# Optimization experiments

Measured on AMD Instinct MI355X. Metric: run time of the kernel, lower is better.

Reference implementation:

```python
import jax, jax.numpy as jnp
import numpy as np

N_NEG = 60
TEMP = 0.07

def _normalize(x, axis):
    n = jnp.sqrt(jnp.sum(x * x, axis=axis, keepdims=True))
    return x / jnp.maximum(n, 1e-12)

def _grid_sample(img, grid):
    # img [B,C,H,W], grid [B,h,w,2] in [-1,1]; bilinear, padding_mode='border', align_corners=False
    B, C, H, W = img.shape
    ix = jnp.clip((grid[..., 0] + 1.0) * (W * 0.5) - 0.5, 0.0, W - 1.0)
    iy = jnp.clip((grid[..., 1] + 1.0) * (H * 0.5) - 0.5, 0.0, H - 1.0)
    x0 = jnp.floor(ix); y0 = jnp.floor(iy)
    x1 = jnp.minimum(x0 + 1.0, W - 1.0); y1 = jnp.minimum(y0 + 1.0, H - 1.0)
    wx = (ix - x0)[:, None]; wy = (iy - y0)[:, None]  # [B,1,h,w]
    imgf = img.reshape(B, C, H * W)
    hh, ww = grid.shape[1], grid.shape[2]
    def gat(yy, xx):
        idx = (yy * W + xx).astype(jnp.int32).reshape(B, 1, hh * ww)
        return jnp.take_along_axis(imgf, idx, axis=2).reshape(B, C, hh, ww)
    v00 = gat(y0, x0); v01 = gat(y0, x1); v10 = gat(y1, x0); v11 = gat(y1, x1)
    return (v00 * (1 - wx) * (1 - wy) + v01 * wx * (1 - wy)
            + v10 * (1 - wx) * wy + v11 * wx * wy)

def _forward(ref_fms, tgt_fms, target_l, target_r, queue):
    b, c, h, w = ref_fms.shape
    s = target_l.shape[-1] // w  # integer downscale factor (nearest interpolate == strided slice)
    disps_l = target_l[:, :, ::s, ::s] / float(s)   # [b,1,h,w]
    disps_r = target_r[:, :, ::s, ::s] / float(s)
    xb = jnp.broadcast_to(jnp.linspace(0.0, 1.0, w), (b, h, w))
    yb = jnp.broadcast_to(jnp.linspace(0.0, 1.0, h)[:, None], (b, h, w))

    def warp(img, disp):
        g = jnp.stack([xb + disp[:, 0] / w, yb], axis=-1)
        return _grid_sample(img, 2.0 * g - 1.0)

    # occlusion / validity mask (detached in the original)
    index = jnp.broadcast_to(jnp.arange(w, dtype=ref_fms.dtype), (b, 1, h, w))
    l2r2l = warp(warp(index, disps_r), -disps_l)
    masko = jnp.abs(index - l2r2l)[:, 0] < 3.0
    mask = masko & (disps_l[:, 0] > 0.0) & (xb - disps_l[:, 0] / w >= 0.0)
    mask = jax.lax.stop_gradient(mask).astype(ref_fms.dtype)  # [b,h,w]

    query = _normalize(ref_fms, 1)
    # positive: warp right feature to left view via disparity
    gpos = jnp.stack([xb - disps_l[:, 0] / w, yb], axis=-1)
    positive = _normalize(_grid_sample(tgt_fms, 2.0 * gpos - 1.0), 1)
    l_pos = jnp.einsum('bchw,bchw->bhw', query, positive)[..., None]

    # negatives: random integer pixel shifts around positive location
    # (no n_neg-fold repeat of tgt_fms; vmap grid_sample over the n axis instead)
    k1, k2 = jax.random.split(jax.random.key(1234))
    mag = jax.random.randint(k1, (b, h, w, N_NEG), 1, 25).astype(ref_fms.dtype)
    sgn = jnp.sign(jax.random.uniform(k2, (b, h, w, N_NEG)) - 0.5).astype(ref_fms.dtype)
    x_right = (xb - disps_l[:, 0] / w) * w
    fx = jnp.mod(x_right[..., None] + mag * sgn, float(w)) / w
    fy = fx / h  # faithful to original code (y coord reuses the normalized x coord)
    grids = jnp.moveaxis(jnp.stack([fx, fy], axis=-1), 3, 0)  # [n,b,h,w,2]
    neg = jax.vmap(lambda g: _grid_sample(tgt_fms, 2.0 * g - 1.0))(grids)  # [n,b,c,h,w]
    neg = _normalize(jnp.moveaxis(neg, 0, -1), 1)  # [b,c,h,w,n]
    l_neg = jnp.einsum('bchw,bchwn->bhwn', query, neg)

    qn = _normalize(queue, 0)  # forward re-normalizes the queue each call
    l_q = jnp.einsum('bchw,ck->bhwk', query, jax.lax.stop_gradient(qn))

    logits = jnp.concatenate([l_pos, l_neg, l_q], axis=-1) * mask[..., None]
    logits = logits.reshape(b * h * w, -1) / TEMP
    # CrossEntropyLoss with all-zero labels (positive is class 0)
    return jnp.mean(-jax.nn.log_softmax(logits, axis=-1)[:, 0])

def setup_inputs():
    key = jax.random.key(0)
    k1, k2, k3, k4, k5 = jax.random.split(key, 5)
    b, c, h, w = 2, 128, 64, 128
    H, W = 4 * h, 4 * w
    return {
        'ref_fms': jax.random.normal(k1, (b, c, h, w), jnp.float32),
        'tgt_fms': jax.random.normal(k2, (b, c, h, w), jnp.float32),
        'target_l': jax.random.uniform(k3, (b, 1, H, W), jnp.float32) * 64.0,
        'target_r': jax.random.uniform(k4, (b, 1, H, W), jnp.float32) * 64.0,
        'queue': jax.random.normal(k5, (c, 6000), jnp.float32),
    }

def reference(ref_fms, tgt_fms, target_l, target_r, queue):
    return _forward(ref_fms, tgt_fms, target_l, target_r, queue)
```

## Files before the change

kernel.cpp:

```cpp
#include <hip/hip_runtime.h>
#include <stdint.h>
#include <math.h>

#define HFM 64
#define WFM 128
#define CFM 128
#define BN 2
#define HWFM (HFM*WFM)
#define NPIX (BN*HWFM)
#define KQ 6000
#define KQP 6144
#define NNEG 60
#define NE (NPIX*NNEG)
#define EHALF_U 491520u
#define MSHIFT 15.0f
#define LOG2E 1.4426950408889634f
#define BSTRIDE 136

typedef _Float16 f16_8 __attribute__((ext_vector_type(8)));
typedef _Float16 f16_2 __attribute__((ext_vector_type(2)));
typedef float f32_4 __attribute__((ext_vector_type(4)));

__host__ __device__ __forceinline__ void threefry2x32(uint32_t k0, uint32_t k1,
                                                      uint32_t x0, uint32_t x1,
                                                      uint32_t* o0, uint32_t* o1) {
  uint32_t ks2 = k0 ^ k1 ^ 0x1BD11BDAu;
  x0 += k0; x1 += k1;
#define TFR(r) { x0 += x1; x1 = (x1 << (r)) | (x1 >> (32 - (r))); x1 ^= x0; }
  TFR(13) TFR(15) TFR(26) TFR(6)
  x0 += k1;  x1 += ks2 + 1u;
  TFR(17) TFR(29) TFR(16) TFR(24)
  x0 += ks2; x1 += k0 + 2u;
  TFR(13) TFR(15) TFR(26) TFR(6)
  x0 += k0;  x1 += k1 + 3u;
  TFR(17) TFR(29) TFR(16) TFR(24)
  x0 += k1;  x1 += ks2 + 4u;
  TFR(13) TFR(15) TFR(26) TFR(6)
  x0 += ks2; x1 += k0 + 5u;
#undef TFR
  *o0 = x0; *o1 = x1;
}

__device__ __forceinline__ void gs_coord(float t, float halfdim, float maxc,
                                         int* i0, int* i1, float* w) {
  float g = 2.0f * t - 1.0f;
  float x = (g + 1.0f) * halfdim - 0.5f;
  x = fminf(fmaxf(x, 0.0f), maxc);
  float f = floorf(x);
  *i0 = (int)f;
  *w = x - f;
  *i1 = (int)fminf(f + 1.0f, maxc);
}

__global__ __launch_bounds__(256) void k_A(
    const float* __restrict__ ref, const float* __restrict__ tgt,
    const float* __restrict__ queue,
    const float* __restrict__ target_l, const float* __restrict__ target_r,
    _Float16* __restrict__ refTf, _Float16* __restrict__ tgtTf,
    _Float16* __restrict__ queueTf, float2* __restrict__ qeb,
    float* __restrict__ maskArr, float* __restrict__ xr) {
  __shared__ float tile[32][33];
  int blk = blockIdx.x;
  int tid = threadIdx.x;
  if (blk < 4096) {
    int z = blk >> 10, yb_ = (blk >> 8) & 3, xb_ = blk & 255;
    int arr = z >> 1, b = z & 1;
    const float* src = (arr == 0 ? ref : tgt) + (size_t)b * CFM * HWFM;
    _Float16* dst = (arr == 0 ? refTf : tgtTf) + (size_t)b * HWFM * CFM;
    int x0 = xb_ * 32, y0 = yb_ * 32;
    int tx = tid & 31, ty = tid >> 5;
#pragma unroll
    for (int i = 0; i < 32; i += 8)
      tile[ty + i][tx] = src[(size_t)(y0 + ty + i) * HWFM + x0 + tx];
    __syncthreads();
#pragma unroll
    for (int i = 0; i < 32; i += 8)
      dst[(size_t)(x0 + ty + i) * CFM + (y0 + tx)] = (_Float16)tile[tx][ty + i];
  } else if (blk < 4864) {
    int q = blk - 4096;
    int cy = q / 192, nx = q - cy * 192;
    int n0 = nx * 32, c0 = cy * 32;
    int tx = tid & 31, ty = tid >> 5;
#pragma unroll
    for (int i = 0; i < 32; i += 8) {
      int n = n0 + tx;
      tile[ty + i][tx] = (n < KQ) ? queue[(size_t)(c0 + ty + i) * KQ + n] : 0.0f;
    }
    __syncthreads();
#pragma unroll
    for (int i = 0; i < 32; i += 8)
      queueTf[(size_t)(n0 + ty + i) * CFM + (c0 + tx)] = (_Float16)tile[tx][ty + i];
  } else if (blk < 4888) {
    int k = (blk - 4864) * 256 + tid;
    if (k < KQP) {
      if (k >= KQ) { qeb[k] = make_float2(0.0f, -1000.0f); }
      else {
        float ss = 0.0f;
        for (int c = 0; c < CFM; c++) { float v = queue[c * KQ + k]; ss += v * v; }
        float qi = 1.0f / fmaxf(sqrtf(ss), 1e-12f);
        qeb[k] = make_float2(qi * (LOG2E / 0.07f), -MSHIFT * LOG2E);
      }
    }
  } else {
    int p = (blk - 4888) * 256 + tid;
    int b = p >> 13;
    int rem = p & (HWFM - 1);
    int i = rem >> 7, j = rem & 127;
    const float stepx = 1.0f / 127.0f, stepy = 1.0f / 63.0f;
    float xb = (j == 127) ? 1.0f : j * stepx;
    float yb = (i == 63) ? 1.0f : i * stepy;
    const float* tl = target_l + (size_t)b * 256 * 512;
    const float* tr = target_r + (size_t)b * 256 * 512;
    float dl = tl[(4 * i) * 512 + 4 * j] * 0.25f;
    int y0i, y1i; float wy;
    gs_coord(yb, 32.0f, 63.0f, &y0i, &y1i, &wy);
    float t = xb - dl * (1.0f / 128.0f);
    int x0i, x1i; float wx;
    gs_coord(t, 64.0f, 127.0f, &x0i, &x1i, &wx);
    auto innerv = [&](int y, int x) -> float {
      float xbx = (x == 127) ? 1.0f : x * stepx;
      float drv = tr[(4 * y) * 512 + 4 * x] * 0.25f;
      float ti = xbx + drv * (1.0f / 128.0f);
      float g = 2.0f * ti - 1.0f;
      float ix2 = fminf(fmaxf((g + 1.0f) * 64.0f - 0.5f, 0.0f), 127.0f);
      float x0f = floorf(ix2);
      float wxp = ix2 - x0f;
      float x1f = fminf(x0f + 1.0f, 127.0f);
      return x0f * (1.0f - wxp) + x1f * wxp;
    };
    float v00 = innerv(y0i, x0i), v01 = innerv(y0i, x1i);
    float v10 = innerv(y1i, x0i), v11 = innerv(y1i, x1i);
    float l2r2l = v00 * (1.0f - wx) * (1.0f - wy) + v01 * wx * (1.0f - wy)
                + v10 * (1.0f - wx) * wy + v11 * wx * wy;
    bool masko = fabsf((float)j - l2r2l) < 3.0f;
    bool mk = masko && (dl > 0.0f) && (t >= 0.0f);
    maskArr[p] = mk ? 1.0f : 0.0f;
    xr[p] = t * 128.0f;
  }
}

__global__ __launch_bounds__(256) void k_compact(const float* __restrict__ maskArr,
                                                 int* __restrict__ count,
                                                 int* __restrict__ list) {
  __shared__ int wsum[4];
  int tid = threadIdx.x;
  int lane = tid & 63, wave = tid >> 6;
  int base_p = tid * 64;
  unsigned long long bits = 0ull;
  const float4* m4 = (const float4*)(maskArr + base_p);
#pragma unroll
  for (int k = 0; k < 16; k++) {
    float4 v = m4[k];
    if (v.x > 0.0f) bits |= 1ull << (4 * k + 0);
    if (v.y > 0.0f) bits |= 1ull << (4 * k + 1);
    if (v.z > 0.0f) bits |= 1ull << (4 * k + 2);
    if (v.w > 0.0f) bits |= 1ull << (4 * k + 3);
  }
  int m = __popcll(bits);
  int scan = m;
#pragma unroll
  for (int off = 1; off < 64; off <<= 1) {
    int n = __shfl_up(scan, off, 64);
    if (lane >= off) scan += n;
  }
  if (lane == 63) wsum[wave] = scan;
  __syncthreads();
  int wbase = 0;
  for (int w = 0; w < wave; w++) wbase += wsum[w];
  int idx = wbase + scan - m;
  for (int k = 0; k < 64; k++) {
    if ((bits >> k) & 1ull) list[idx++] = base_p + k;
  }
  if (tid == 255) *count = idx;
}

__global__ __launch_bounds__(256) void k_B(
    const _Float16* __restrict__ refTf, const _Float16* __restrict__ tgtTf,
    _Float16* __restrict__ QTfc, float* __restrict__ stats,
    const float* __restrict__ maskArr, const float* __restrict__ xr,
    float* __restrict__ S, float* __restrict__ logit0,
    const int* __restrict__ count, const int* __restrict__ list) {
  int blk = blockIdx.x;
  int tid = threadIdx.x;
  int lane = tid & 63;
  if (blk < 64) {
    int sub = tid >> 6;
    int xg = blk * 4 + sub;
    int b = xg >> 7, x = xg & 127;
    int xp = min(x + 1, 127);
    int c2 = lane * 2;
    int base = b * HWFM;
    f16_2 c0  = *(const f16_2*)(tgtTf + (size_t)(base + x) * CFM + c2);
    f16_2 c1  = *(const f16_2*)(tgtTf + (size_t)(base + WFM + x) * CFM + c2);
    f16_2 c0p = *(const f16_2*)(tgtTf + (size_t)(base + xp) * CFM + c2);
    f16_2 c1p = *(const f16_2*)(tgtTf + (size_t)(base + WFM + xp) * CFM + c2);
    float a0 = (float)c0[0], a1 = (float)c0[1];
    float b0 = (float)c1[0], b1 = (float)c1[1];
    float p0 = (float)c0p[0], p1 = (float)c0p[1];
    float q0 = (float)c1p[0], q1 = (float)c1p[1];
    float s[7];
    s[0] = a0 * a0 + a1 * a1;
    s[1] = a0 * b0 + a1 * b1;
    s[2] = b0 * b0 + b1 * b1;
    s[3] = a0 * p0 + a1 * p1;
    s[4] = a0 * q0 + a1 * q1;
    s[5] = b0 * p0 + b1 * p1;
    s[6] = b0 * q0 + b1 * q1;
#pragma unroll
    for (int o = 32; o; o >>= 1)
#pragma unroll
      for (int k = 0; k < 7; k++) s[k] += __shfl_xor(s[k], o, 64);
    if (lane == 0) {
      float* st = stats + (size_t)xg * 8;
#pragma unroll
      for (int k = 0; k < 7; k++) st[k] = s[k];
      st[7] = 0.0f;
    }
  } else {
    int wave = tid >> 6;
    int cnt = *count;
    int slot = (blk - 64) * 4 + wave;
    if (slot >= cnt) return;
    int p = list[slot];
    int b = p >> 13;
    int rem = p & (HWFM - 1);
    int i = rem >> 7;
    const float stepy = 1.0f / 63.0f;
    float yb = (i == 63) ? 1.0f : i * stepy;
    float t = xr[p] * (1.0f / 128.0f);
    int y0i, y1i; float wy;
    gs_coord(yb, 32.0f, 63.0f, &y0i, &y1i, &wy);
    int x0i, x1i; float wx;
    gs_coord(t, 64.0f, 127.0f, &x0i, &x1i, &wx);

    int c2 = lane * 2;
    f16_2 q2 = *(const f16_2*)(refTf + (size_t)p * CFM + c2);
    int bo = b * HWFM;
    f16_2 a2 = *(const f16_2*)(tgtTf + (size_t)(bo + y0i * WFM + x0i) * CFM + c2);
    f16_2 b2 = *(const f16_2*)(tgtTf + (size_t)(bo + y0i * WFM + x1i) * CFM + c2);
    f16_2 cc2 = *(const f16_2*)(tgtTf + (size_t)(bo + y1i * WFM + x0i) * CFM + c2);
    f16_2 d2 = *(const f16_2*)(tgtTf + (size_t)(bo + y1i * WFM + x1i) * CFM + c2);

    float w00 = (1.0f - wx) * (1.0f - wy), w01 = wx * (1.0f - wy);
    float w10 = (1.0f - wx) * wy,          w11 = wx * wy;
    float q0 = (float)q2[0], q1 = (float)q2[1];
    float v0 = w00 * (float)a2[0] + w01 * (float)b2[0] + w10 * (float)cc2[0] + w11 * (float)d2[0];
    float v1 = w00 * (float)a2[1] + w01 * (float)b2[1] + w10 * (float)cc2[1] + w11 * (float)d2[1];

    float s0 = q0 * q0 + q1 * q1;
    float s1 = q0 * v0 + q1 * v1;
    float s2 = v0 * v0 + v1 * v1;
#pragma unroll
    for (int o = 32; o; o >>= 1) {
      s0 += __shfl_xor(s0, o, 64);
      s1 += __shfl_xor(s1, o, 64);
      s2 += __shfl_xor(s2, o, 64);
    }
    float inv = 1.0f / fmaxf(sqrtf(s0), 1e-12f);
    f16_2 qw; qw[0] = (_Float16)(q0 * inv); qw[1] = (_Float16)(q1 * inv);
    *(f16_2*)(QTfc + (size_t)slot * CFM + c2) = qw;
    if (lane == 0) {
      float lpos = (s1 * inv) / fmaxf(sqrtf(s2), 1e-12f);
      float lg0 = lpos / 0.07f;
      logit0[p] = lg0;
      S[p] = expf(lg0 - MSHIFT);
    }
  }
}

__global__ __launch_bounds__(256) void k_gemm(
    const _Float16* __restrict__ QTfc,
    const _Float16* __restrict__ queueTf,
    const _Float16* __restrict__ tgtTf,
    const float2* __restrict__ qeb,
    float* __restrict__ S, float* __restrict__ D,
    const int* __restrict__ count, const int* __restrict__ list) {
  __shared__ _Float16 Bs[128 * BSTRIDE];
  __shared__ float Srow[64];
  __shared__ int pb[64];
  int tid = threadIdx.x;
  int cnt = *count;
  int pblk = blockIdx.y * 64;
  if (pblk >= cnt) return;
  int wave = tid >> 6, lane = tid & 63;
  int quad = lane >> 4, l16 = lane & 15;
  int wm = wave >> 1, wn = wave & 1;

  if (tid < 64) {
    Srow[tid] = 0.0f;
    pb[tid] = list[min(pblk + tid, cnt - 1)] >> 13;
  }

  f16_8 Af[2][4];
  int r0 = pblk + wm * 32;
#pragma unroll
  for (int mt = 0; mt < 2; mt++) {
    const _Float16* arow = QTfc + (size_t)min(r0 + mt * 16 + l16, cnt - 1) * CFM + quad * 8;
#pragma unroll
    for (int ks = 0; ks < 4; ks++)
      Af[mt][ks] = *(const f16_8*)(arow + ks * 32);
  }

  if (blockIdx.x < 4) {
    int batch = blockIdx.x >> 1;
    const _Float16* bsrc = tgtTf + ((size_t)batch * HWFM + (blockIdx.x & 1) * 128) * CFM;
#pragma unroll
    for (int it = 0; it < 8; it++) {
      int idx = it * 256 + tid;
      int row = idx >> 4, c16 = idx & 15;
      *(f16_8*)(&Bs[row * BSTRIDE + c16 * 8]) =
          *(const f16_8*)(bsrc + (size_t)row * CFM + c16 * 8);
    }
    __syncthreads();

    f32_4 acc[2][4];
#pragma unroll
    for (int mt = 0; mt < 2; mt++)
#pragma unroll
      for (int nt = 0; nt < 4; nt++)
        acc[mt][nt] = (f32_4){0.0f, 0.0f, 0.0f, 0.0f};
#pragma unroll
    for (int ks = 0; ks < 4; ks++) {
      f16_8 Bk[4];
#pragma unroll
      for (int nt = 0; nt < 4; nt++)
        Bk[nt] = *(const f16_8*)(&Bs[(wn * 64 + nt * 16 + l16) * BSTRIDE + ks * 32 + quad * 8]);
#pragma unroll
      for (int mt = 0; mt < 2; mt++)
#pragma unroll
        for (int nt = 0; nt < 4; nt++)
          acc[mt][nt] = __builtin_amdgcn_mfma_f32_16x16x32_f16(Af[mt][ks], Bk[nt], acc[mt][nt], 0, 0, 0);
    }
#pragma unroll
    for (int mt = 0; mt < 2; mt++)
#pragma unroll
      for (int nt = 0; nt < 4; nt++)
#pragma unroll
        for (int r = 0; r < 4; r++) {
          int rowloc = wm * 32 + mt * 16 + quad * 4 + r;
          int slot = pblk + rowloc;
          int colL = (blockIdx.x & 1) * 128 + wn * 64 + nt * 16 + l16;
          if (slot < cnt && pb[rowloc] == batch)
            D[(size_t)slot * 256 + colL] = acc[mt][nt][r];
        }
    __syncthreads();
  }

  float rowsum[2][4] = {{0.0f,0.0f,0.0f,0.0f},{0.0f,0.0f,0.0f,0.0f}};
#pragma unroll
  for (int ic = 0; ic < 4; ic++) {
    int n0 = (blockIdx.x * 4 + ic) * 128;
    {
      const _Float16* bsrc = queueTf + (size_t)n0 * CFM;
#pragma unroll
      for (int it = 0; it < 8; it++) {
        int idx = it * 256 + tid;
        int row = idx >> 4, c16 = idx & 15;
        *(f16_8*)(&Bs[row * BSTRIDE + c16 * 8]) =
            *(const f16_8*)(bsrc + (size_t)row * CFM + c16 * 8);
      }
    }
    float2 qb[4];
#pragma unroll
    for (int nt = 0; nt < 4; nt++) qb[nt] = qeb[n0 + wn * 64 + nt * 16 + l16];
    __syncthreads();

    f32_4 acc[2][4];
#pragma unroll
    for (int mt = 0; mt < 2; mt++)
#pragma unroll
      for (int nt = 0; nt < 4; nt++)
        acc[mt][nt] = (f32_4){0.0f, 0.0f, 0.0f, 0.0f};
#pragma unroll
    for (int ks = 0; ks < 4; ks++) {
      f16_8 Bk[4];
#pragma unroll
      for (int nt = 0; nt < 4; nt++)
        Bk[nt] = *(const f16_8*)(&Bs[(wn * 64 + nt * 16 + l16) * BSTRIDE + ks * 32 + quad * 8]);
#pragma unroll
      for (int mt = 0; mt < 2; mt++)
#pragma unroll
        for (int nt = 0; nt < 4; nt++)
          acc[mt][nt] = __builtin_amdgcn_mfma_f32_16x16x32_f16(Af[mt][ks], Bk[nt], acc[mt][nt], 0, 0, 0);
    }
#pragma unroll
    for (int nt = 0; nt < 4; nt++)
#pragma unroll
      for (int mt = 0; mt < 2; mt++)
#pragma unroll
        for (int r = 0; r < 4; r++)
          rowsum[mt][r] += exp2f(fmaf(acc[mt][nt][r], qb[nt].x, qb[nt].y));
    __syncthreads();
  }

#pragma unroll
  for (int mt = 0; mt < 2; mt++)
#pragma unroll
    for (int r = 0; r < 4; r++) {
      float vv = rowsum[mt][r];
      vv += __shfl_xor(vv, 1);
      vv += __shfl_xor(vv, 2);
      vv += __shfl_xor(vv, 4);
      vv += __shfl_xor(vv, 8);
      rowsum[mt][r] = vv;
    }
  if (l16 == 0) {
#pragma unroll
    for (int mt = 0; mt < 2; mt++)
#pragma unroll
      for (int r = 0; r < 4; r++)
        atomicAdd(&Srow[wm * 32 + mt * 16 + quad * 4 + r], rowsum[mt][r]);
  }
  __syncthreads();
  if (tid < 64) {
    int pr = pblk + tid;
    if (pr < cnt) atomicAdd(&S[list[pr]], Srow[tid]);
  }
}

__global__ __launch_bounds__(256) void k_negatives_lite(
    const float* __restrict__ D, const float* __restrict__ stats,
    const float* __restrict__ xr, float* __restrict__ S,
    const int* __restrict__ count, const int* __restrict__ list,
    uint32_t k1a, uint32_t k1b, uint32_t k2a, uint32_t k2b) {
  int tid = threadIdx.x;
  int wave = tid >> 6, lane = tid & 63;
  int cnt = *count;
  int slot = blockIdx.x * 4 + wave;
  if (slot >= cnt) return;
  int p = list[slot];
  int b = p >> 13;
  float esum = 0.0f;
  if (lane < NNEG) {
    uint32_t e = (uint32_t)(p * NNEG + lane);
    uint32_t h0, h1;
    threefry2x32(k1a, k1b, e, e + (uint32_t)NE, &h0, &h1);
    uint32_t off = ((h0 % 24u) * 16u + (h1 % 24u)) % 24u;
    float mag = (float)(1u + off);
    uint32_t ub;
    {
      uint32_t a, bm;
      if (e < EHALF_U) { threefry2x32(k2a, k2b, e, e + EHALF_U, &a, &bm); ub = a; }
      else             { threefry2x32(k2a, k2b, e - EHALF_U, e, &a, &bm); ub = bm; }
    }
    float u = __uint_as_float((ub >> 9) | 0x3F800000u) - 1.0f;
    float sg = (u > 0.5f) ? 1.0f : ((u < 0.5f) ? -1.0f : 0.0f);

    float v = xr[p] + mag * sg;
    float r = fmodf(v, 128.0f);
    if (r < 0.0f) r += 128.0f;
    float fx = r * (1.0f / 128.0f);
    float fy = fx * (1.0f / 64.0f);
    int x0i, x1i, y0i, y1i; float wx, wy;
    gs_coord(fx, 64.0f, 127.0f, &x0i, &x1i, &wx);
    gs_coord(fy, 32.0f, 63.0f, &y0i, &y1i, &wy);

    const float* Dp = D + (size_t)slot * 256;
    float d00 = Dp[x0i], d01 = Dp[x1i];
    float d10 = Dp[128 + x0i], d11 = Dp[128 + x1i];
    float u0 = 1.0f - wy, u1 = wy;
    float dv0 = u0 * d00 + u1 * d10;
    float dv1 = u0 * d01 + u1 * d11;
    float dot = (1.0f - wx) * dv0 + wx * dv1;

    const float* st0 = stats + (size_t)(b * 128 + x0i) * 8;
    const float* st1 = stats + (size_t)(b * 128 + x1i) * 8;
    float4 sa = *(const float4*)st0;
    float4 sb = *(const float4*)(st0 + 4);
    float4 sc = *(const float4*)st1;
    float a0 = u0 * u0, a1 = u0 * u1, a2 = u1 * u1;
    float nB0 = a0 * sa.x + 2.0f * a1 * sa.y + a2 * sa.z;
    float nB1 = a0 * sc.x + 2.0f * a1 * sc.y + a2 * sc.z;
    float cB  = a0 * sa.w + a1 * (sb.x + sb.y) + a2 * sb.z;
    float wx0 = 1.0f - wx;
    float nsq = wx0 * wx0 * nB0 + 2.0f * wx * wx0 * cB + wx * wx * nB1;
    float ln = dot / fmaxf(sqrtf(fmaxf(nsq, 0.0f)), 1e-12f);
    esum = __expf(ln * (1.0f / 0.07f) - MSHIFT);
  }
#pragma unroll
  for (int o = 32; o; o >>= 1) esum += __shfl_xor(esum, o, 64);
  if (lane == 0) atomicAdd(&S[p], esum);
}

__global__ __launch_bounds__(1024) void k_finalize(
    const float* __restrict__ S, const float* __restrict__ logit0,
    const float* __restrict__ maskArr, float* __restrict__ out) {
  int tid = threadIdx.x;
  const float cmask = logf(6061.0f);
  double acc = 0.0;
  for (int p = tid; p < NPIX; p += 1024) {
    float term = (maskArr[p] > 0.0f) ? (logf(S[p]) + MSHIFT - logit0[p]) : cmask;
    acc += (double)term;
  }
#pragma unroll
  for (int off = 32; off; off >>= 1) acc += __shfl_down(acc, off, 64);
  __shared__ double sd[16];
  if ((tid & 63) == 0) sd[tid >> 6] = acc;
  __syncthreads();
  if (tid == 0) {
    double tot = 0.0;
    for (int w = 0; w < 16; w++) tot += sd[w];
    out[0] = (float)(tot / (double)NPIX);
  }
}

extern "C" void kernel_launch(void* const* d_in, const int* in_sizes, int n_in,
                              void* d_out, int out_size, void* d_ws, size_t ws_size,
                              hipStream_t stream) {
  const float* ref   = (const float*)d_in[0];
  const float* tgt   = (const float*)d_in[1];
  const float* tl    = (const float*)d_in[2];
  const float* tr    = (const float*)d_in[3];
  const float* queue = (const float*)d_in[4];
  float* out = (float*)d_out;
  float* ws = (float*)d_ws;

  float2* qeb = (float2*)ws;
  float* S    = ws + 12288;
  float* lg0  = ws + 28672;
  float* mk   = ws + 45056;
  float* xr   = ws + 61440;
  int* count  = (int*)(ws + 77824);
  int* list   = (int*)(ws + 77840);
  _Float16* QTfc    = (_Float16*)(ws + 94464);
  _Float16* queueTf = (_Float16*)(ws + 1143040);
  _Float16* tgtTf   = (_Float16*)(ws + 1536256);
  _Float16* refTf   = (_Float16*)(ws + 2584832);
  float* stats = ws + 3633408;
  float* D     = ws + 3635456;

  uint32_t b0o0, b0o1, b1o0, b1o1;
  threefry2x32(0u, 1234u, 0u, 2u, &b0o0, &b0o1);
  threefry2x32(0u, 1234u, 1u, 3u, &b1o0, &b1o1);
  uint32_t k1a = b0o0, k1b = b1o0, k2a = b0o1, k2b = b1o1;

  k_A<<<dim3(4952), dim3(256), 0, stream>>>(ref, tgt, queue, tl, tr,
                                            refTf, tgtTf, queueTf, qeb, mk, xr);
  k_compact<<<dim3(1), dim3(256), 0, stream>>>(mk, count, list);
  k_B<<<dim3(64 + 4096), dim3(256), 0, stream>>>(refTf, tgtTf, QTfc, stats,
                                                 mk, xr, S, lg0, count, list);
  k_gemm<<<dim3(12, NPIX / 64), dim3(256), 0, stream>>>(QTfc, queueTf, tgtTf, qeb,
                                                        S, D, count, list);
  k_negatives_lite<<<dim3(NPIX / 4), dim3(256), 0, stream>>>(D, stats, xr, S, count, list,
                                                             k1a, k1b, k2a, k2b);
  k_finalize<<<dim3(1), dim3(1024), 0, stream>>>(S, lg0, mk, out);
}
```

Measured before the change: 137.4 us.

## Double-buffer queue tiles in GEMM, fold compaction into k_B, halve GEMM grid

The queue GEMM now prefetches the next 128-column B tile into registers while running MFMAs on the current tile, then writes it into a second LDS buffer. This removes one barrier per iteration and hides global-load latency. Each block now covers 8 chunks instead of 4, so the grid is halved. The separate compaction kernel is merged into k_B as block 0, and the normalized query rows are written per pixel using the mask directly. The GEMM then gathers its A rows through the list. In exchange, LDS use doubles, register pressure rises, there are fewer GEMM blocks for occupancy, and the A-row reads become indirect.

```diff
diff --git a/kernel.cpp b/kernel.cpp
--- a/kernel.cpp
+++ b/kernel.cpp
@@ -62,47 +62,8 @@
   __shared__ float tile[32][33];
   int blk = blockIdx.x;
   int tid = threadIdx.x;
-  if (blk < 4096) {
-    int z = blk >> 10, yb_ = (blk >> 8) & 3, xb_ = blk & 255;
-    int arr = z >> 1, b = z & 1;
-    const float* src = (arr == 0 ? ref : tgt) + (size_t)b * CFM * HWFM;
-    _Float16* dst = (arr == 0 ? refTf : tgtTf) + (size_t)b * HWFM * CFM;
-    int x0 = xb_ * 32, y0 = yb_ * 32;
-    int tx = tid & 31, ty = tid >> 5;
-#pragma unroll
-    for (int i = 0; i < 32; i += 8)
-      tile[ty + i][tx] = src[(size_t)(y0 + ty + i) * HWFM + x0 + tx];
-    __syncthreads();
-#pragma unroll
-    for (int i = 0; i < 32; i += 8)
-      dst[(size_t)(x0 + ty + i) * CFM + (y0 + tx)] = (_Float16)tile[tx][ty + i];
-  } else if (blk < 4864) {
-    int q = blk - 4096;
-    int cy = q / 192, nx = q - cy * 192;
-    int n0 = nx * 32, c0 = cy * 32;
-    int tx = tid & 31, ty = tid >> 5;
-#pragma unroll
-    for (int i = 0; i < 32; i += 8) {
-      int n = n0 + tx;
-      tile[ty + i][tx] = (n < KQ) ? queue[(size_t)(c0 + ty + i) * KQ + n] : 0.0f;
-    }
-    __syncthreads();
-#pragma unroll
-    for (int i = 0; i < 32; i += 8)
-      queueTf[(size_t)(n0 + ty + i) * CFM + (c0 + tx)] = (_Float16)tile[tx][ty + i];
-  } else if (blk < 4888) {
-    int k = (blk - 4864) * 256 + tid;
-    if (k < KQP) {
-      if (k >= KQ) { qeb[k] = make_float2(0.0f, -1000.0f); }
-      else {
-        float ss = 0.0f;
-        for (int c = 0; c < CFM; c++) { float v = queue[c * KQ + k]; ss += v * v; }
-        float qi = 1.0f / fmaxf(sqrtf(ss), 1e-12f);
-        qeb[k] = make_float2(qi * (LOG2E / 0.07f), -MSHIFT * LOG2E);
-      }
-    }
-  } else {
-    int p = (blk - 4888) * 256 + tid;
+  if (blk < 64) {
+    int p = blk * 256 + tid;
     int b = p >> 13;
     int rem = p & (HWFM - 1);
     int i = rem >> 7, j = rem & 127;
@@ -136,56 +97,91 @@
     bool mk = masko && (dl > 0.0f) && (t >= 0.0f);
     maskArr[p] = mk ? 1.0f : 0.0f;
     xr[p] = t * 128.0f;
-  }
-}
-
-__global__ __launch_bounds__(256) void k_compact(const float* __restrict__ maskArr,
-                                                 int* __restrict__ count,
-                                                 int* __restrict__ list) {
-  __shared__ int wsum[4];
-  int tid = threadIdx.x;
-  int lane = tid & 63, wave = tid >> 6;
-  int base_p = tid * 64;
-  unsigned long long bits = 0ull;
-  const float4* m4 = (const float4*)(maskArr + base_p);
-#pragma unroll
-  for (int k = 0; k < 16; k++) {
-    float4 v = m4[k];
-    if (v.x > 0.0f) bits |= 1ull << (4 * k + 0);
-    if (v.y > 0.0f) bits |= 1ull << (4 * k + 1);
-    if (v.z > 0.0f) bits |= 1ull << (4 * k + 2);
-    if (v.w > 0.0f) bits |= 1ull << (4 * k + 3);
-  }
-  int m = __popcll(bits);
-  int scan = m;
-#pragma unroll
-  for (int off = 1; off < 64; off <<= 1) {
-    int n = __shfl_up(scan, off, 64);
-    if (lane >= off) scan += n;
-  }
-  if (lane == 63) wsum[wave] = scan;
-  __syncthreads();
-  int wbase = 0;
-  for (int w = 0; w < wave; w++) wbase += wsum[w];
-  int idx = wbase + scan - m;
-  for (int k = 0; k < 64; k++) {
-    if ((bits >> k) & 1ull) list[idx++] = base_p + k;
-  }
-  if (tid == 255) *count = idx;
+  } else if (blk < 88) {
+    int k = (blk - 64) * 256 + tid;
+    if (k < KQP) {
+      if (k >= KQ) { qeb[k] = make_float2(0.0f, -1000.0f); }
+      else {
+        float ss = 0.0f;
+        for (int c = 0; c < CFM; c++) { float v = queue[c * KQ + k]; ss += v * v; }
+        float qi = 1.0f / fmaxf(sqrtf(ss), 1e-12f);
+        qeb[k] = make_float2(qi * (LOG2E / 0.07f), -MSHIFT * LOG2E);
+      }
+    }
+  } else if (blk < 856) {
+    int q = blk - 88;
+    int cy = q / 192, nx = q - cy * 192;
+    int n0 = nx * 32, c0 = cy * 32;
+    int tx = tid & 31, ty = tid >> 5;
+#pragma unroll
+    for (int i = 0; i < 32; i += 8) {
+      int n = n0 + tx;
+      tile[ty + i][tx] = (n < KQ) ? queue[(size_t)(c0 + ty + i) * KQ + n] : 0.0f;
+    }
+    __syncthreads();
+#pragma unroll
+    for (int i = 0; i < 32; i += 8)
+      queueTf[(size_t)(n0 + ty + i) * CFM + (c0 + tx)] = (_Float16)tile[tx][ty + i];
+  } else {
+    int fblk = blk - 856;
+    int z = fblk >> 10, yb_ = (fblk >> 8) & 3, xb_ = fblk & 255;
+    int arr = z >> 1, b = z & 1;
+    const float* src = (arr == 0 ? ref : tgt) + (size_t)b * CFM * HWFM;
+    _Float16* dst = (arr == 0 ? refTf : tgtTf) + (size_t)b * HWFM * CFM;
+    int x0 = xb_ * 32, y0 = yb_ * 32;
+    int tx = tid & 31, ty = tid >> 5;
+#pragma unroll
+    for (int i = 0; i < 32; i += 8)
+      tile[ty + i][tx] = src[(size_t)(y0 + ty + i) * HWFM + x0 + tx];
+    __syncthreads();
+#pragma unroll
+    for (int i = 0; i < 32; i += 8)
+      dst[(size_t)(x0 + ty + i) * CFM + (y0 + tx)] = (_Float16)tile[tx][ty + i];
+  }
 }
 
 __global__ __launch_bounds__(256) void k_B(
     const _Float16* __restrict__ refTf, const _Float16* __restrict__ tgtTf,
-    _Float16* __restrict__ QTfc, float* __restrict__ stats,
+    _Float16* __restrict__ QTf, float* __restrict__ stats,
     const float* __restrict__ maskArr, const float* __restrict__ xr,
     float* __restrict__ S, float* __restrict__ logit0,
-    const int* __restrict__ count, const int* __restrict__ list) {
+    int* __restrict__ count, int* __restrict__ list) {
+  __shared__ int wsum[4];
   int blk = blockIdx.x;
   int tid = threadIdx.x;
   int lane = tid & 63;
-  if (blk < 64) {
+  if (blk == 0) {
+    int wave = tid >> 6;
+    int base_p = tid * 64;
+    unsigned long long bits = 0ull;
+    const float4* m4 = (const float4*)(maskArr + base_p);
+#pragma unroll
+    for (int k = 0; k < 16; k++) {
+      float4 v = m4[k];
+      if (v.x > 0.0f) bits |= 1ull << (4 * k + 0);
+      if (v.y > 0.0f) bits |= 1ull << (4 * k + 1);
+      if (v.z > 0.0f) bits |= 1ull << (4 * k + 2);
+      if (v.w > 0.0f) bits |= 1ull << (4 * k + 3);
+    }
+    int m = __popcll(bits);
+    int scan = m;
+#pragma unroll
+    for (int off = 1; off < 64; off <<= 1) {
+      int n = __shfl_up(scan, off, 64);
+      if (lane >= off) scan += n;
+    }
+    if (lane == 63) wsum[wave] = scan;
+    __syncthreads();
+    int wbase = 0;
+    for (int w = 0; w < wave; w++) wbase += wsum[w];
+    int idx = wbase + scan - m;
+    for (int k = 0; k < 64; k++) {
+      if ((bits >> k) & 1ull) list[idx++] = base_p + k;
+    }
+    if (tid == 255) *count = idx;
+  } else if (blk < 65) {
     int sub = tid >> 6;
-    int xg = blk * 4 + sub;
+    int xg = (blk - 1) * 4 + sub;
     int b = xg >> 7, x = xg & 127;
     int xp = min(x + 1, 127);
     int c2 = lane * 2;
@@ -218,10 +214,9 @@
     }
   } else {
     int wave = tid >> 6;
-    int cnt = *count;
-    int slot = (blk - 64) * 4 + wave;
-    if (slot >= cnt) return;
-    int p = list[slot];
+    int p = (blk - 65) * 4 + wave;
+    float mk = maskArr[p];
+    if (mk == 0.0f) return;
     int b = p >> 13;
     int rem = p & (HWFM - 1);
     int i = rem >> 7;
@@ -258,7 +253,7 @@
     }
     float inv = 1.0f / fmaxf(sqrtf(s0), 1e-12f);
     f16_2 qw; qw[0] = (_Float16)(q0 * inv); qw[1] = (_Float16)(q1 * inv);
-    *(f16_2*)(QTfc + (size_t)slot * CFM + c2) = qw;
+    *(f16_2*)(QTf + (size_t)p * CFM + c2) = qw;
     if (lane == 0) {
       float lpos = (s1 * inv) / fmaxf(sqrtf(s2), 1e-12f);
       float lg0 = lpos / 0.07f;
@@ -269,13 +264,13 @@
 }
 
 __global__ __launch_bounds__(256) void k_gemm(
-    const _Float16* __restrict__ QTfc,
+    const _Float16* __restrict__ QTf,
     const _Float16* __restrict__ queueTf,
     const _Float16* __restrict__ tgtTf,
     const float2* __restrict__ qeb,
     float* __restrict__ S, float* __restrict__ D,
     const int* __restrict__ count, const int* __restrict__ list) {
-  __shared__ _Float16 Bs[128 * BSTRIDE];
+  __shared__ _Float16 Bs[2][128 * BSTRIDE];
   __shared__ float Srow[64];
   __shared__ int pb[64];
   int tid = threadIdx.x;
@@ -295,24 +290,41 @@
   int r0 = pblk + wm * 32;
 #pragma unroll
   for (int mt = 0; mt < 2; mt++) {
-    const _Float16* arow = QTfc + (size_t)min(r0 + mt * 16 + l16, cnt - 1) * CFM + quad * 8;
+    int prow = list[min(r0 + mt * 16 + l16, cnt - 1)];
+    const _Float16* arow = QTf + (size_t)prow * CFM + quad * 8;
 #pragma unroll
     for (int ks = 0; ks < 4; ks++)
       Af[mt][ks] = *(const f16_8*)(arow + ks * 32);
   }
 
+  f16_8 sreg[8];
+  int srow[8], sc16[8];
+#pragma unroll
+  for (int it = 0; it < 8; it++) {
+    int idx = it * 256 + tid;
+    srow[it] = idx >> 4; sc16[it] = idx & 15;
+  }
+  auto load_src = [&](const _Float16* bsrc) {
+#pragma unroll
+    for (int it = 0; it < 8; it++)
+      sreg[it] = *(const f16_8*)(bsrc + (size_t)srow[it] * CFM + sc16[it] * 8);
+  };
+  auto write_lds = [&](int buf) {
+#pragma unroll
+    for (int it = 0; it < 8; it++)
+      *(f16_8*)(&Bs[buf][srow[it] * BSTRIDE + sc16[it] * 8]) = sreg[it];
+  };
+
+  int nbase = blockIdx.x * 8 * 128;
+  int cur;
+  float rowsum[2][4] = {{0.0f,0.0f,0.0f,0.0f},{0.0f,0.0f,0.0f,0.0f}};
+
   if (blockIdx.x < 4) {
     int batch = blockIdx.x >> 1;
-    const _Float16* bsrc = tgtTf + ((size_t)batch * HWFM + (blockIdx.x & 1) * 128) * CFM;
-#pragma unroll
-    for (int it = 0; it < 8; it++) {
-      int idx = it * 256 + tid;
-      int row = idx >> 4, c16 = idx & 15;
-      *(f16_8*)(&Bs[row * BSTRIDE + c16 * 8]) =
-          *(const f16_8*)(bsrc + (size_t)row * CFM + c16 * 8);
-    }
-    __syncthreads();
-
+    load_src(tgtTf + ((size_t)batch * HWFM + (blockIdx.x & 1) * 128) * CFM);
+    write_lds(0);
+    __syncthreads();
+    load_src(queueTf + (size_t)nbase * CFM);
     f32_4 acc[2][4];
 #pragma unroll
     for (int mt = 0; mt < 2; mt++)
@@ -324,7 +336,7 @@
       f16_8 Bk[4];
 #pragma unroll
       for (int nt = 0; nt < 4; nt++)
-        Bk[nt] = *(const f16_8*)(&Bs[(wn * 64 + nt * 16 + l16) * BSTRIDE + ks * 32 + quad * 8]);
+        Bk[nt] = *(const f16_8*)(&Bs[0][(wn * 64 + nt * 16 + l16) * BSTRIDE + ks * 32 + quad * 8]);
 #pragma unroll
       for (int mt = 0; mt < 2; mt++)
 #pragma unroll
@@ -343,27 +355,23 @@
           if (slot < cnt && pb[rowloc] == batch)
             D[(size_t)slot * 256 + colL] = acc[mt][nt][r];
         }
-    __syncthreads();
-  }
-
-  float rowsum[2][4] = {{0.0f,0.0f,0.0f,0.0f},{0.0f,0.0f,0.0f,0.0f}};
-#pragma unroll
-  for (int ic = 0; ic < 4; ic++) {
-    int n0 = (blockIdx.x * 4 + ic) * 128;
-    {
-      const _Float16* bsrc = queueTf + (size_t)n0 * CFM;
-#pragma unroll
-      for (int it = 0; it < 8; it++) {
-        int idx = it * 256 + tid;
-        int row = idx >> 4, c16 = idx & 15;
-        *(f16_8*)(&Bs[row * BSTRIDE + c16 * 8]) =
-            *(const f16_8*)(bsrc + (size_t)row * CFM + c16 * 8);
-      }
-    }
+    write_lds(1);
+    __syncthreads();
+    cur = 1;
+  } else {
+    load_src(queueTf + (size_t)nbase * CFM);
+    write_lds(0);
+    __syncthreads();
+    cur = 0;
+  }
+
+#pragma unroll
+  for (int ic = 0; ic < 8; ic++) {
+    int n0 = nbase + ic * 128;
+    if (ic + 1 < 8) load_src(queueTf + (size_t)(n0 + 128) * CFM);
     float2 qb[4];
 #pragma unroll
     for (int nt = 0; nt < 4; nt++) qb[nt] = qeb[n0 + wn * 64 + nt * 16 + l16];
-    __syncthreads();
 
     f32_4 acc[2][4];
 #pragma unroll
@@ -376,13 +384,15 @@
       f16_8 Bk[4];
 #pragma unroll
       for (int nt = 0; nt < 4; nt++)
-        Bk[nt] = *(const f16_8*)(&Bs[(wn * 64 + nt * 16 + l16) * BSTRIDE + ks * 32 + quad * 8]);
+        Bk[nt] = *(const f16_8*)(&Bs[cur][(wn * 64 + nt * 16 + l16) * BSTRIDE + ks * 32 + quad * 8]);
 #pragma unroll
       for (int mt = 0; mt < 2; mt++)
 #pragma unroll
         for (int nt = 0; nt < 4; nt++)
           acc[mt][nt] = __builtin_amdgcn_mfma_f32_16x16x32_f16(Af[mt][ks], Bk[nt], acc[mt][nt], 0, 0, 0);
     }
+    if (ic + 1 < 8) write_lds(cur ^ 1);
+
 #pragma unroll
     for (int nt = 0; nt < 4; nt++)
 #pragma unroll
@@ -391,6 +401,7 @@
         for (int r = 0; r < 4; r++)
           rowsum[mt][r] += exp2f(fmaf(acc[mt][nt][r], qb[nt].x, qb[nt].y));
     __syncthreads();
+    cur ^= 1;
   }
 
 #pragma unroll
@@ -522,7 +533,7 @@
   float* xr   = ws + 61440;
   int* count  = (int*)(ws + 77824);
   int* list   = (int*)(ws + 77840);
-  _Float16* QTfc    = (_Float16*)(ws + 94464);
+  _Float16* QTf     = (_Float16*)(ws + 94464);
   _Float16* queueTf = (_Float16*)(ws + 1143040);
   _Float16* tgtTf   = (_Float16*)(ws + 1536256);
   _Float16* refTf   = (_Float16*)(ws + 2584832);
@@ -536,11 +547,10 @@
 
   k_A<<<dim3(4952), dim3(256), 0, stream>>>(ref, tgt, queue, tl, tr,
                                             refTf, tgtTf, queueTf, qeb, mk, xr);
-  k_compact<<<dim3(1), dim3(256), 0, stream>>>(mk, count, list);
-  k_B<<<dim3(64 + 4096), dim3(256), 0, stream>>>(refTf, tgtTf, QTfc, stats,
+  k_B<<<dim3(65 + 4096), dim3(256), 0, stream>>>(refTf, tgtTf, QTf, stats,
                                                  mk, xr, S, lg0, count, list);
-  k_gemm<<<dim3(12, NPIX / 64), dim3(256), 0, stream>>>(QTfc, queueTf, tgtTf, qeb,
-                                                        S, D, count, list);
+  k_gemm<<<dim3(6, NPIX / 64), dim3(256), 0, stream>>>(QTf, queueTf, tgtTf, qeb,
+                                                       S, D, count, list);
   k_negatives_lite<<<dim3(NPIX / 4), dim3(256), 0, stream>>>(D, stats, xr, S, count, list,
                                                              k1a, k1b, k2a, k2b);
   k_finalize<<<dim3(1), dim3(1024), 0, stream>>>(S, lg0, mk, out);
```

After: 130.8 us. 4.8% less time.

## Prefetch GEMM B tiles into registers, store D in fp16, reorder k_A blocks

Applied to the files above, without the earlier changes.

Inside the GEMM kernel, the next 128-column queue tile is loaded from global memory into registers while the current tile is being computed, and then written to LDS. This is meant to hide load latency behind the MFMA work. The intermediate D matrix is now written and read as fp16, halving its traffic between the GEMM and the negatives kernel at some cost in precision. In k_A the small mask and queue-norm blocks are moved ahead of the transposes so they start first, and an unused mask argument is removed from k_B.

```diff
diff --git a/kernel.cpp b/kernel.cpp
--- a/kernel.cpp
+++ b/kernel.cpp
@@ -62,47 +62,8 @@
   __shared__ float tile[32][33];
   int blk = blockIdx.x;
   int tid = threadIdx.x;
-  if (blk < 4096) {
-    int z = blk >> 10, yb_ = (blk >> 8) & 3, xb_ = blk & 255;
-    int arr = z >> 1, b = z & 1;
-    const float* src = (arr == 0 ? ref : tgt) + (size_t)b * CFM * HWFM;
-    _Float16* dst = (arr == 0 ? refTf : tgtTf) + (size_t)b * HWFM * CFM;
-    int x0 = xb_ * 32, y0 = yb_ * 32;
-    int tx = tid & 31, ty = tid >> 5;
-#pragma unroll
-    for (int i = 0; i < 32; i += 8)
-      tile[ty + i][tx] = src[(size_t)(y0 + ty + i) * HWFM + x0 + tx];
-    __syncthreads();
-#pragma unroll
-    for (int i = 0; i < 32; i += 8)
-      dst[(size_t)(x0 + ty + i) * CFM + (y0 + tx)] = (_Float16)tile[tx][ty + i];
-  } else if (blk < 4864) {
-    int q = blk - 4096;
-    int cy = q / 192, nx = q - cy * 192;
-    int n0 = nx * 32, c0 = cy * 32;
-    int tx = tid & 31, ty = tid >> 5;
-#pragma unroll
-    for (int i = 0; i < 32; i += 8) {
-      int n = n0 + tx;
-      tile[ty + i][tx] = (n < KQ) ? queue[(size_t)(c0 + ty + i) * KQ + n] : 0.0f;
-    }
-    __syncthreads();
-#pragma unroll
-    for (int i = 0; i < 32; i += 8)
-      queueTf[(size_t)(n0 + ty + i) * CFM + (c0 + tx)] = (_Float16)tile[tx][ty + i];
-  } else if (blk < 4888) {
-    int k = (blk - 4864) * 256 + tid;
-    if (k < KQP) {
-      if (k >= KQ) { qeb[k] = make_float2(0.0f, -1000.0f); }
-      else {
-        float ss = 0.0f;
-        for (int c = 0; c < CFM; c++) { float v = queue[c * KQ + k]; ss += v * v; }
-        float qi = 1.0f / fmaxf(sqrtf(ss), 1e-12f);
-        qeb[k] = make_float2(qi * (LOG2E / 0.07f), -MSHIFT * LOG2E);
-      }
-    }
-  } else {
-    int p = (blk - 4888) * 256 + tid;
+  if (blk < 64) {
+    int p = blk * 256 + tid;
     int b = p >> 13;
     int rem = p & (HWFM - 1);
     int i = rem >> 7, j = rem & 127;
@@ -136,6 +97,46 @@
     bool mk = masko && (dl > 0.0f) && (t >= 0.0f);
     maskArr[p] = mk ? 1.0f : 0.0f;
     xr[p] = t * 128.0f;
+  } else if (blk < 88) {
+    int k = (blk - 64) * 256 + tid;
+    if (k < KQP) {
+      if (k >= KQ) { qeb[k] = make_float2(0.0f, -1000.0f); }
+      else {
+        float ss = 0.0f;
+        for (int c = 0; c < CFM; c++) { float v = queue[c * KQ + k]; ss += v * v; }
+        float qi = 1.0f / fmaxf(sqrtf(ss), 1e-12f);
+        qeb[k] = make_float2(qi * (LOG2E / 0.07f), -MSHIFT * LOG2E);
+      }
+    }
+  } else if (blk < 856) {
+    int q = blk - 88;
+    int cy = q / 192, nx = q - cy * 192;
+    int n0 = nx * 32, c0 = cy * 32;
+    int tx = tid & 31, ty = tid >> 5;
+#pragma unroll
+    for (int i = 0; i < 32; i += 8) {
+      int n = n0 + tx;
+      tile[ty + i][tx] = (n < KQ) ? queue[(size_t)(c0 + ty + i) * KQ + n] : 0.0f;
+    }
+    __syncthreads();
+#pragma unroll
+    for (int i = 0; i < 32; i += 8)
+      queueTf[(size_t)(n0 + ty + i) * CFM + (c0 + tx)] = (_Float16)tile[tx][ty + i];
+  } else {
+    int fblk = blk - 856;
+    int z = fblk >> 10, yb_ = (fblk >> 8) & 3, xb_ = fblk & 255;
+    int arr = z >> 1, b = z & 1;
+    const float* src = (arr == 0 ? ref : tgt) + (size_t)b * CFM * HWFM;
+    _Float16* dst = (arr == 0 ? refTf : tgtTf) + (size_t)b * HWFM * CFM;
+    int x0 = xb_ * 32, y0 = yb_ * 32;
+    int tx = tid & 31, ty = tid >> 5;
+#pragma unroll
+    for (int i = 0; i < 32; i += 8)
+      tile[ty + i][tx] = src[(size_t)(y0 + ty + i) * HWFM + x0 + tx];
+    __syncthreads();
+#pragma unroll
+    for (int i = 0; i < 32; i += 8)
+      dst[(size_t)(x0 + ty + i) * CFM + (y0 + tx)] = (_Float16)tile[tx][ty + i];
   }
 }
 
@@ -177,7 +178,7 @@
 __global__ __launch_bounds__(256) void k_B(
     const _Float16* __restrict__ refTf, const _Float16* __restrict__ tgtTf,
     _Float16* __restrict__ QTfc, float* __restrict__ stats,
-    const float* __restrict__ maskArr, const float* __restrict__ xr,
+    const float* __restrict__ xr,
     float* __restrict__ S, float* __restrict__ logit0,
     const int* __restrict__ count, const int* __restrict__ list) {
   int blk = blockIdx.x;
@@ -273,7 +274,7 @@
     const _Float16* __restrict__ queueTf,
     const _Float16* __restrict__ tgtTf,
     const float2* __restrict__ qeb,
-    float* __restrict__ S, float* __restrict__ D,
+    float* __restrict__ S, _Float16* __restrict__ Dh,
     const int* __restrict__ count, const int* __restrict__ list) {
   __shared__ _Float16 Bs[128 * BSTRIDE];
   __shared__ float Srow[64];
@@ -301,18 +302,40 @@
       Af[mt][ks] = *(const f16_8*)(arow + ks * 32);
   }
 
-  if (blockIdx.x < 4) {
+  f16_8 sreg[8];
+  int srow[8], sc16[8];
+#pragma unroll
+  for (int it = 0; it < 8; it++) {
+    int idx = it * 256 + tid;
+    srow[it] = idx >> 4; sc16[it] = idx & 15;
+  }
+  auto load_src = [&](const _Float16* bsrc) {
+#pragma unroll
+    for (int it = 0; it < 8; it++)
+      sreg[it] = *(const f16_8*)(bsrc + (size_t)srow[it] * CFM + sc16[it] * 8);
+  };
+  auto write_lds = [&]() {
+#pragma unroll
+    for (int it = 0; it < 8; it++)
+      *(f16_8*)(&Bs[srow[it] * BSTRIDE + sc16[it] * 8]) = sreg[it];
+  };
+
+  int nbase = blockIdx.x * 4 * 128;
+  bool hasD = blockIdx.x < 4;
+  float rowsum[2][4] = {{0.0f,0.0f,0.0f,0.0f},{0.0f,0.0f,0.0f,0.0f}};
+
+  if (hasD) {
     int batch = blockIdx.x >> 1;
-    const _Float16* bsrc = tgtTf + ((size_t)batch * HWFM + (blockIdx.x & 1) * 128) * CFM;
-#pragma unroll
-    for (int it = 0; it < 8; it++) {
-      int idx = it * 256 + tid;
-      int row = idx >> 4, c16 = idx & 15;
-      *(f16_8*)(&Bs[row * BSTRIDE + c16 * 8]) =
-          *(const f16_8*)(bsrc + (size_t)row * CFM + c16 * 8);
-    }
+    load_src(tgtTf + ((size_t)batch * HWFM + (blockIdx.x & 1) * 128) * CFM);
+  } else {
+    load_src(queueTf + (size_t)nbase * CFM);
+  }
+
+  if (hasD) {
+    write_lds();
     __syncthreads();
-
+    load_src(queueTf + (size_t)nbase * CFM);
+    int batch = blockIdx.x >> 1;
     f32_4 acc[2][4];
 #pragma unroll
     for (int mt = 0; mt < 2; mt++)
@@ -341,29 +364,20 @@
           int slot = pblk + rowloc;
           int colL = (blockIdx.x & 1) * 128 + wn * 64 + nt * 16 + l16;
           if (slot < cnt && pb[rowloc] == batch)
-            D[(size_t)slot * 256 + colL] = acc[mt][nt][r];
+            Dh[(size_t)slot * 256 + colL] = (_Float16)acc[mt][nt][r];
         }
     __syncthreads();
   }
 
-  float rowsum[2][4] = {{0.0f,0.0f,0.0f,0.0f},{0.0f,0.0f,0.0f,0.0f}};
 #pragma unroll
   for (int ic = 0; ic < 4; ic++) {
-    int n0 = (blockIdx.x * 4 + ic) * 128;
-    {
-      const _Float16* bsrc = queueTf + (size_t)n0 * CFM;
-#pragma unroll
-      for (int it = 0; it < 8; it++) {
-        int idx = it * 256 + tid;
-        int row = idx >> 4, c16 = idx & 15;
-        *(f16_8*)(&Bs[row * BSTRIDE + c16 * 8]) =
-            *(const f16_8*)(bsrc + (size_t)row * CFM + c16 * 8);
-      }
-    }
+    int n0 = nbase + ic * 128;
+    write_lds();
+    __syncthreads();
+    if (ic < 3) load_src(queueTf + (size_t)(n0 + 128) * CFM);
     float2 qb[4];
 #pragma unroll
     for (int nt = 0; nt < 4; nt++) qb[nt] = qeb[n0 + wn * 64 + nt * 16 + l16];
-    __syncthreads();
 
     f32_4 acc[2][4];
 #pragma unroll
@@ -419,7 +433,7 @@
 }
 
 __global__ __launch_bounds__(256) void k_negatives_lite(
-    const float* __restrict__ D, const float* __restrict__ stats,
+    const _Float16* __restrict__ Dh, const float* __restrict__ stats,
     const float* __restrict__ xr, float* __restrict__ S,
     const int* __restrict__ count, const int* __restrict__ list,
     uint32_t k1a, uint32_t k1b, uint32_t k2a, uint32_t k2b) {
@@ -455,9 +469,9 @@
     gs_coord(fx, 64.0f, 127.0f, &x0i, &x1i, &wx);
     gs_coord(fy, 32.0f, 63.0f, &y0i, &y1i, &wy);
 
-    const float* Dp = D + (size_t)slot * 256;
-    float d00 = Dp[x0i], d01 = Dp[x1i];
-    float d10 = Dp[128 + x0i], d11 = Dp[128 + x1i];
+    const _Float16* Dp = Dh + (size_t)slot * 256;
+    float d00 = (float)Dp[x0i], d01 = (float)Dp[x1i];
+    float d10 = (float)Dp[128 + x0i], d11 = (float)Dp[128 + x1i];
     float u0 = 1.0f - wy, u1 = wy;
     float dv0 = u0 * d00 + u1 * d10;
     float dv1 = u0 * d01 + u1 * d11;
@@ -527,7 +541,7 @@
   _Float16* tgtTf   = (_Float16*)(ws + 1536256);
   _Float16* refTf   = (_Float16*)(ws + 2584832);
   float* stats = ws + 3633408;
-  float* D     = ws + 3635456;
+  _Float16* Dh = (_Float16*)(ws + 3635456);
 
   uint32_t b0o0, b0o1, b1o0, b1o1;
   threefry2x32(0u, 1234u, 0u, 2u, &b0o0, &b0o1);
@@ -538,10 +552,10 @@
                                             refTf, tgtTf, queueTf, qeb, mk, xr);
   k_compact<<<dim3(1), dim3(256), 0, stream>>>(mk, count, list);
   k_B<<<dim3(64 + 4096), dim3(256), 0, stream>>>(refTf, tgtTf, QTfc, stats,
-                                                 mk, xr, S, lg0, count, list);
+                                                 xr, S, lg0, count, list);
   k_gemm<<<dim3(12, NPIX / 64), dim3(256), 0, stream>>>(QTfc, queueTf, tgtTf, qeb,
-                                                        S, D, count, list);
-  k_negatives_lite<<<dim3(NPIX / 4), dim3(256), 0, stream>>>(D, stats, xr, S, count, list,
+                                                        S, Dh, count, list);
+  k_negatives_lite<<<dim3(NPIX / 4), dim3(256), 0, stream>>>(Dh, stats, xr, S, count, list,
                                                              k1a, k1b, k2a, k2b);
   k_finalize<<<dim3(1), dim3(1024), 0, stream>>>(S, lg0, mk, out);
 }
```

After: 133.0 us. 1.03x faster.
